# Kernel tuning notes

Measured on AMD Instinct MI355X. Metric: run time of the kernel, lower is better.

Reference implementation:

```python
import jax, jax.numpy as jnp
import numpy as np

N, C, W, H = 16, 64, 512, 512
RED, OUT_W = 64, 128
BN_EPS = 1e-5


def setup_inputs() -> dict:
    key = jax.random.key(0)
    ks = jax.random.split(key, 5)
    x = jax.random.normal(ks[0], (N, C, W, H), dtype=jnp.float32)
    w1 = jax.random.normal(ks[1], (RED, W), dtype=jnp.float32) * (1.0 / np.sqrt(W))
    b1 = jax.random.normal(ks[2], (RED,), dtype=jnp.float32) * 0.01
    gamma = jnp.ones((RED,), dtype=jnp.float32)
    beta = jnp.zeros((RED,), dtype=jnp.float32)
    w2 = jax.random.normal(ks[3], (W, RED), dtype=jnp.float32) * (1.0 / np.sqrt(RED))
    b2 = jax.random.normal(ks[4], (W,), dtype=jnp.float32) * 0.01
    return {"x": x, "w1": w1, "b1": b1, "gamma": gamma, "beta": beta, "w2": w2, "b2": b2}


def reference(x, w1, b1, gamma, beta, w2, b2):
    # attention_dim == 2: permute(0,2,1,3) -> [N,W,C,H]; AdaptiveMaxPool2d((1,1))
    # over (C,H) == global max over axes (1,3) of original x -> [N, W]
    pooled = jnp.max(x, axis=(1, 3))                       # [N, W]
    # Linear(W -> RED)
    h = pooled @ w1.T + b1                                 # [N, RED]
    # BatchNorm1d in training mode: batch stats (biased variance)
    mu = jnp.mean(h, axis=0)
    var = jnp.mean((h - mu) ** 2, axis=0)
    h = gamma * (h - mu) * jax.lax.rsqrt(var + BN_EPS) + beta
    h = jax.nn.relu(h)
    # Linear(RED -> W) + softmax over width
    att = jax.nn.softmax(h @ w2.T + b2, axis=1)            # [N, W]
    # topk over width, then sort selected indices ascending
    _, idx = jax.lax.top_k(att, OUT_W)                     # [N, OUT_W]
    idx = jnp.sort(idx, axis=1)
    # batched gather along width axis: x[i, :, idx[i], :]
    return jnp.take_along_axis(x, idx[:, None, :, None], axis=2)  # [N, C, OUT_W, H]
```

## Files before the change

kernel.cpp:

```cpp
#include <hip/hip_runtime.h>
#include <cstdint>
#include <math.h>

#define Nn   16
#define Cc   64
#define Ww   512
#define Hh   512
#define RED  64
#define OUTW 128

__global__ void __launch_bounds__(256) pool_kernel(const float* __restrict__ x,
                                                   float* __restrict__ pooled) {
    const int b = blockIdx.x;
    const int n = b >> 7;
    const int q = b & 127;
    const int r = threadIdx.x >> 6;
    const int lane = threadIdx.x & 63;
    const int w = q * 4 + r;
    const float* base = x + ((size_t)n * Cc * Ww + w) * Hh + lane * 8;

    float m0 = -INFINITY, m1 = -INFINITY, m2 = -INFINITY, m3 = -INFINITY;
    float m4 = -INFINITY, m5 = -INFINITY, m6 = -INFINITY, m7 = -INFINITY;
    #pragma unroll 4
    for (int c = 0; c < Cc; ++c) {
        const float* p = base + (size_t)c * (Ww * Hh);
        const float4 v0 = *reinterpret_cast<const float4*>(p);
        const float4 v1 = *reinterpret_cast<const float4*>(p + 4);
        m0 = fmaxf(m0, v0.x); m1 = fmaxf(m1, v0.y);
        m2 = fmaxf(m2, v0.z); m3 = fmaxf(m3, v0.w);
        m4 = fmaxf(m4, v1.x); m5 = fmaxf(m5, v1.y);
        m6 = fmaxf(m6, v1.z); m7 = fmaxf(m7, v1.w);
    }
    float m = fmaxf(fmaxf(fmaxf(m0, m1), fmaxf(m2, m3)),
                    fmaxf(fmaxf(m4, m5), fmaxf(m6, m7)));
    #pragma unroll
    for (int off = 1; off < 64; off <<= 1)
        m = fmaxf(m, __shfl_xor(m, off, 64));
    if (lane == 0) pooled[n * Ww + w] = m;
}

__global__ void __launch_bounds__(512) mlp_topk_kernel(
    const float* __restrict__ pooled,
    const float* __restrict__ w1,
    const float* __restrict__ b1,
    const float* __restrict__ gamma,
    const float* __restrict__ beta,
    const float* __restrict__ w2,
    const float* __restrict__ b2,
    int* __restrict__ idx_out)
{
    const int row = blockIdx.x;
    const int tid = threadIdx.x;

    __shared__ float pooled_t[Ww][Nn + 1];
    __shared__ float hbn_t[RED][Nn + 1];
    __shared__ float mu_s[RED], is_s[RED];
    __shared__ float logits_row[Ww];
    __shared__ unsigned long long sel_mask[Ww / 64];

    for (int i = tid; i < Nn * Ww; i += 512) {
        const int n = i >> 9, k = i & 511;
        pooled_t[k][n] = pooled[i];
    }
    __syncthreads();

    float hv[2];
    int hn[2], hr[2];
    #pragma unroll
    for (int e = 0; e < 2; ++e) {
        const int item = e * 512 + tid;
        const int n = item & 15, r = item >> 4;
        hn[e] = n; hr[e] = r;
        float acc = b1[r];
        for (int k = 0; k < Ww; ++k)
            acc += pooled_t[k][n] * w1[r * Ww + k];
        hv[e] = acc;
    }
    #pragma unroll
    for (int e = 0; e < 2; ++e) hbn_t[hr[e]][hn[e]] = hv[e];
    __syncthreads();

    if (tid < RED) {
        float s = 0.f, s2 = 0.f;
        #pragma unroll
        for (int n = 0; n < Nn; ++n) { const float v = hbn_t[tid][n]; s += v; s2 += v * v; }
        const float mu  = s  * (1.f / Nn);
        const float var = s2 * (1.f / Nn) - mu * mu;
        mu_s[tid] = mu;
        is_s[tid] = 1.f / sqrtf(var + 1e-5f);
    }
    __syncthreads();

    #pragma unroll
    for (int e = 0; e < 2; ++e) {
        const int r = hr[e], n = hn[e];
        const float v = gamma[r] * (hv[e] - mu_s[r]) * is_s[r] + beta[r];
        hbn_t[r][n] = fmaxf(v, 0.f);
    }
    __syncthreads();

    {
        const int w = tid;
        float acc = b2[w];
        #pragma unroll
        for (int r = 0; r < RED; ++r)
            acc += hbn_t[r][row] * w2[w * RED + r];
        logits_row[w] = acc;
    }
    __syncthreads();

    {
        const int w = tid;
        const float v = logits_row[w];
        int rank = 0;
        for (int ww = 0; ww < Ww; ++ww) {
            const float u = logits_row[ww];
            rank += (u > v || (u == v && ww < w)) ? 1 : 0;
        }
        const bool sel = (rank < OUTW);
        const unsigned long long m = __ballot(sel);
        if ((tid & 63) == 0) sel_mask[tid >> 6] = m;
        __syncthreads();
        if (sel) {
            int pos = 0;
            #pragma unroll
            for (int bb = 0; bb < (Ww / 64); ++bb)
                if (bb < (w >> 6)) pos += __popcll(sel_mask[bb]);
            pos += __popcll(sel_mask[w >> 6] & ((1ULL << (w & 63)) - 1ULL));
            idx_out[row * OUTW + pos] = w;
        }
    }
}

__global__ void __launch_bounds__(256) gather_kernel(const float* __restrict__ x,
                                                     const int* __restrict__ idx,
                                                     float* __restrict__ out) {
    const int b = blockIdx.x;
    const int n = b >> 6;
    const int tid = threadIdx.x;
    __shared__ int sidx[OUTW];
    if (tid < OUTW) sidx[tid] = idx[n * OUTW + tid];
    __syncthreads();
    const float* src = x   + (size_t)b * (Ww * Hh);
    float*       dst = out + (size_t)b * (OUTW * Hh);
    #pragma unroll 4
    for (int i = tid; i < OUTW * (Hh / 4); i += 256) {
        const int j = i >> 7;
        const int f = i & 127;
        const float4 v = *reinterpret_cast<const float4*>(src + (size_t)sidx[j] * Hh + f * 4);
        *reinterpret_cast<float4*>(dst + (size_t)j * Hh + f * 4) = v;
    }
}

extern "C" void kernel_launch(void* const* d_in, const int* in_sizes, int n_in,
                              void* d_out, int out_size, void* d_ws, size_t ws_size,
                              hipStream_t stream) {
    const float* x     = (const float*)d_in[0];
    const float* w1    = (const float*)d_in[1];
    const float* b1    = (const float*)d_in[2];
    const float* gamma = (const float*)d_in[3];
    const float* beta  = (const float*)d_in[4];
    const float* w2    = (const float*)d_in[5];
    const float* b2    = (const float*)d_in[6];
    float* out = (float*)d_out;

    float* pooled = (float*)d_ws;
    int*   idx    = (int*)((char*)d_ws + Nn * Ww * sizeof(float));

    pool_kernel<<<Nn * (Ww / 4), 256, 0, stream>>>(x, pooled);
    mlp_topk_kernel<<<Nn, 512, 0, stream>>>(pooled, w1, b1, gamma, beta, w2, b2, idx);
    gather_kernel<<<Nn * Cc, 256, 0, stream>>>(x, idx, out);
}
```

Before: 345.0 us.

## Split MLP into per-feature Linear1+BN kernel and separate logits/top-k kernel

The single 16-block MLP/top-k kernel is split in two. The first kernel runs 64 blocks, one per hidden feature, and computes the Linear1 dot products with float4 loads plus the BatchNorm statistics via shuffles. The second kernel keeps w2 rows in registers and does the logits and rank-based top-k. This removes the redundant per-block recomputation of the whole first layer and the serial 512-long loops, at the cost of an extra kernel launch and a workspace round trip.

```diff
diff --git a/kernel.cpp b/kernel.cpp
--- a/kernel.cpp
+++ b/kernel.cpp
@@ -39,96 +39,95 @@
     if (lane == 0) pooled[n * Ww + w] = m;
 }
 
-__global__ void __launch_bounds__(512) mlp_topk_kernel(
+__global__ void __launch_bounds__(256) mlp_h_kernel(
     const float* __restrict__ pooled,
     const float* __restrict__ w1,
     const float* __restrict__ b1,
     const float* __restrict__ gamma,
     const float* __restrict__ beta,
+    float* __restrict__ hbn)
+{
+    const int r = blockIdx.x;
+    const int t = threadIdx.x;
+    const int n = t & 15;
+    const int slice = t >> 4;
+    const float4* w1r = reinterpret_cast<const float4*>(w1 + r * Ww + slice * 32);
+    const float4* pn  = reinterpret_cast<const float4*>(pooled + n * Ww + slice * 32);
+
+    float acc = 0.f;
+    #pragma unroll
+    for (int j = 0; j < 8; ++j) {
+        const float4 a = w1r[j];
+        const float4 p = pn[j];
+        acc += a.x * p.x + a.y * p.y + a.z * p.z + a.w * p.w;
+    }
+    __shared__ float part[16][17];
+    part[slice][n] = acc;
+    __syncthreads();
+    if (t < 16) {
+        float h = b1[r];
+        #pragma unroll
+        for (int s = 0; s < 16; ++s) h += part[s][t];
+        float sum = h, sq = h * h;
+        #pragma unroll
+        for (int off = 1; off < 16; off <<= 1) {
+            sum += __shfl_xor(sum, off, 64);
+            sq  += __shfl_xor(sq,  off, 64);
+        }
+        const float mu  = sum * (1.f / 16.f);
+        const float var = sq  * (1.f / 16.f) - mu * mu;
+        const float is  = 1.f / sqrtf(var + 1e-5f);
+        const float v   = gamma[r] * (h - mu) * is + beta[r];
+        hbn[r * Nn + t] = fmaxf(v, 0.f);
+    }
+}
+
+__global__ void __launch_bounds__(512) logits_topk_kernel(
+    const float* __restrict__ hbn,
     const float* __restrict__ w2,
     const float* __restrict__ b2,
     int* __restrict__ idx_out)
 {
     const int row = blockIdx.x;
-    const int tid = threadIdx.x;
+    const int w = threadIdx.x;
 
-    __shared__ float pooled_t[Ww][Nn + 1];
-    __shared__ float hbn_t[RED][Nn + 1];
-    __shared__ float mu_s[RED], is_s[RED];
+    __shared__ float hrow[RED];
     __shared__ float logits_row[Ww];
     __shared__ unsigned long long sel_mask[Ww / 64];
 
-    for (int i = tid; i < Nn * Ww; i += 512) {
-        const int n = i >> 9, k = i & 511;
-        pooled_t[k][n] = pooled[i];
-    }
+    float4 wv[16];
+    const float4* w2r = reinterpret_cast<const float4*>(w2 + w * RED);
+    #pragma unroll
+    for (int j = 0; j < 16; ++j) wv[j] = w2r[j];
+    if (w < RED) hrow[w] = hbn[w * Nn + row];
     __syncthreads();
 
-    float hv[2];
-    int hn[2], hr[2];
+    float acc = b2[w];
     #pragma unroll
-    for (int e = 0; e < 2; ++e) {
-        const int item = e * 512 + tid;
-        const int n = item & 15, r = item >> 4;
-        hn[e] = n; hr[e] = r;
-        float acc = b1[r];
-        for (int k = 0; k < Ww; ++k)
-            acc += pooled_t[k][n] * w1[r * Ww + k];
-        hv[e] = acc;
+    for (int j = 0; j < 16; ++j) {
+        acc += wv[j].x * hrow[j * 4]     + wv[j].y * hrow[j * 4 + 1]
+             + wv[j].z * hrow[j * 4 + 2] + wv[j].w * hrow[j * 4 + 3];
     }
-    #pragma unroll
-    for (int e = 0; e < 2; ++e) hbn_t[hr[e]][hn[e]] = hv[e];
+    logits_row[w] = acc;
     __syncthreads();
 
-    if (tid < RED) {
-        float s = 0.f, s2 = 0.f;
+    const float v = logits_row[w];
+    int rank = 0;
+    for (int ww = 0; ww < Ww; ++ww) {
+        const float u = logits_row[ww];
+        rank += (u > v || (u == v && ww < w)) ? 1 : 0;
+    }
+    const bool sel = (rank < OUTW);
+    const unsigned long long m = __ballot(sel);
+    if ((w & 63) == 0) sel_mask[w >> 6] = m;
+    __syncthreads();
+    if (sel) {
+        int pos = 0;
         #pragma unroll
-        for (int n = 0; n < Nn; ++n) { const float v = hbn_t[tid][n]; s += v; s2 += v * v; }
-        const float mu  = s  * (1.f / Nn);
-        const float var = s2 * (1.f / Nn) - mu * mu;
-        mu_s[tid] = mu;
-        is_s[tid] = 1.f / sqrtf(var + 1e-5f);
-    }
-    __syncthreads();
-
-    #pragma unroll
-    for (int e = 0; e < 2; ++e) {
-        const int r = hr[e], n = hn[e];
-        const float v = gamma[r] * (hv[e] - mu_s[r]) * is_s[r] + beta[r];
-        hbn_t[r][n] = fmaxf(v, 0.f);
-    }
-    __syncthreads();
-
-    {
-        const int w = tid;
-        float acc = b2[w];
-        #pragma unroll
-        for (int r = 0; r < RED; ++r)
-            acc += hbn_t[r][row] * w2[w * RED + r];
-        logits_row[w] = acc;
-    }
-    __syncthreads();
-
-    {
-        const int w = tid;
-        const float v = logits_row[w];
-        int rank = 0;
-        for (int ww = 0; ww < Ww; ++ww) {
-            const float u = logits_row[ww];
-            rank += (u > v || (u == v && ww < w)) ? 1 : 0;
-        }
-        const bool sel = (rank < OUTW);
-        const unsigned long long m = __ballot(sel);
-        if ((tid & 63) == 0) sel_mask[tid >> 6] = m;
-        __syncthreads();
-        if (sel) {
-            int pos = 0;
-            #pragma unroll
-            for (int bb = 0; bb < (Ww / 64); ++bb)
-                if (bb < (w >> 6)) pos += __popcll(sel_mask[bb]);
-            pos += __popcll(sel_mask[w >> 6] & ((1ULL << (w & 63)) - 1ULL));
-            idx_out[row * OUTW + pos] = w;
-        }
+        for (int bb = 0; bb < (Ww / 64); ++bb)
+            if (bb < (w >> 6)) pos += __popcll(sel_mask[bb]);
+        pos += __popcll(sel_mask[w >> 6] & ((1ULL << (w & 63)) - 1ULL));
+        idx_out[row * OUTW + pos] = w;
     }
 }
 
@@ -165,9 +164,11 @@
     float* out = (float*)d_out;
 
     float* pooled = (float*)d_ws;
-    int*   idx    = (int*)((char*)d_ws + Nn * Ww * sizeof(float));
+    float* hbn    = (float*)((char*)d_ws + 32768);
+    int*   idx    = (int*)((char*)d_ws + 32768 + 4096);
 
     pool_kernel<<<Nn * (Ww / 4), 256, 0, stream>>>(x, pooled);
-    mlp_topk_kernel<<<Nn, 512, 0, stream>>>(pooled, w1, b1, gamma, beta, w2, b2, idx);
+    mlp_h_kernel<<<RED, 256, 0, stream>>>(pooled, w1, b1, gamma, beta, hbn);
+    logits_topk_kernel<<<Nn, 512, 0, stream>>>(hbn, w2, b2, idx);
     gather_kernel<<<Nn * Cc, 256, 0, stream>>>(x, idx, out);
 }
```

New measurement: 323.0 us. -6.4%, faster.
